# Kernel tuning notes

Measured on AMD Instinct MI355X. Metric: run time of the kernel, lower is better.

## Reference

```python
import jax, jax.numpy as jnp
import numpy as np

N_NODES = 100000
N_EDGES = 1000000
D = 64
HID = 64
OUT = 64
N_CLS = 10
N_GRAPHS = 512
BN_EPS = 1e-5


def setup_inputs() -> dict:
    key = jax.random.key(0)
    ks = jax.random.split(key, 16)
    inp = {
        "x": jax.random.normal(ks[0], (N_NODES, D), dtype=jnp.float32),
        "edge_index": jax.random.randint(ks[1], (2, N_EDGES), 0, N_NODES, dtype=jnp.int32),
        "batch": jnp.sort(jax.random.randint(ks[2], (N_NODES,), 0, N_GRAPHS, dtype=jnp.int32)),
    }
    def lin(k, fi, fo):
        lim = 1.0 / np.sqrt(fi)
        kw, kb = jax.random.split(k)
        return (jax.random.uniform(kw, (fi, fo), minval=-lim, maxval=lim, dtype=jnp.float32),
                jax.random.uniform(kb, (fo,), minval=-lim, maxval=lim, dtype=jnp.float32))
    # conv0 MLP([64,64,64]) with BN after first linear
    inp["w0a"], inp["b0a"] = lin(ks[3], D, HID)
    inp["g0"] = jnp.ones((HID,), jnp.float32); inp["be0"] = jnp.zeros((HID,), jnp.float32)
    inp["m0"] = jnp.zeros((HID,), jnp.float32); inp["v0"] = jnp.ones((HID,), jnp.float32)
    inp["w0b"], inp["b0b"] = lin(ks[4], HID, HID)
    # conv1 MLP([64,64,64])
    inp["w1a"], inp["b1a"] = lin(ks[5], HID, HID)
    inp["g1"] = jnp.ones((HID,), jnp.float32); inp["be1"] = jnp.zeros((HID,), jnp.float32)
    inp["m1"] = jnp.zeros((HID,), jnp.float32); inp["v1"] = jnp.ones((HID,), jnp.float32)
    inp["w1b"], inp["b1b"] = lin(ks[6], HID, OUT)
    # classifier
    inp["wc"], inp["bc"] = lin(ks[7], OUT, N_CLS)
    return inp


def _bn_eval(h, g, b, m, v):
    return (h - m) * jax.lax.rsqrt(v + BN_EPS) * g + b


def _mlp(h, wa, ba, g, be, m, v, wb, bb):
    # Linear -> BN -> ReLU -> (dropout eval=identity) -> Linear
    h = h @ wa + ba
    h = jax.nn.relu(_bn_eval(h, g, be, m, v))
    return h @ wb + bb


def _gin_conv(h, src, dst, wa, ba, g, be, m, v, wb, bb):
    # GINConv eps=0: mlp(x + sum_{j->i} x_j), messages scatter-added at dst
    agg = jax.ops.segment_sum(h[src], dst, num_segments=N_NODES)
    return _mlp(h + agg, wa, ba, g, be, m, v, wb, bb)


def reference(x, edge_index, batch,
              w0a, b0a, g0, be0, m0, v0, w0b, b0b,
              w1a, b1a, g1, be1, m1, v1, w1b, b1b,
              wc, bc):
    src, dst = edge_index[0], edge_index[1]
    h = _gin_conv(x, src, dst, w0a, b0a, g0, be0, m0, v0, w0b, b0b)
    h = jax.nn.relu(h)  # dropout is identity in eval
    h = _gin_conv(h, src, dst, w1a, b1a, g1, be1, m1, v1, w1b, b1b)
    # global mean pool over batch indices
    sums = jax.ops.segment_sum(h, batch, num_segments=N_GRAPHS)
    cnts = jax.ops.segment_sum(jnp.ones((h.shape[0],), h.dtype), batch, num_segments=N_GRAPHS)
    pooled = sums / jnp.maximum(cnts, 1.0)[:, None]
    return pooled @ wc + bc
```

## Files before the change

kernel.cpp:

```cpp
#include <hip/hip_runtime.h>

#define N_NODES 100000
#define N_EDGES 1000000
#define N_GRAPHS 512
#define N_CLS 10
#define BN_EPS 1e-5f

#define SCAN_NB 200
#define NTILES 1563

typedef _Float16 half8 __attribute__((ext_vector_type(8)));
typedef _Float16 half4v __attribute__((ext_vector_type(4)));
typedef float floatx4 __attribute__((ext_vector_type(4)));
typedef int intx4 __attribute__((ext_vector_type(4)));

__global__ __launch_bounds__(256) void prep_kernel(
    const float* __restrict__ x, _Float16* __restrict__ xh,
    const int* __restrict__ batch, const int* __restrict__ dstI,
    int* __restrict__ deg, int* __restrict__ rank,
    const float* __restrict__ w0a, const float* __restrict__ b0a,
    const float* __restrict__ g0, const float* __restrict__ be0,
    const float* __restrict__ m0, const float* __restrict__ v0,
    const float* __restrict__ w0b,
    const float* __restrict__ w1a, const float* __restrict__ b1a,
    const float* __restrict__ g1, const float* __restrict__ be1,
    const float* __restrict__ m1, const float* __restrict__ v1,
    const float* __restrict__ w1b,
    int* __restrict__ gstart,
    _Float16* __restrict__ wHi, _Float16* __restrict__ wLo,
    float* __restrict__ b1p0, float* __restrict__ b1p1) {
    const int gid = blockIdx.x * 256 + threadIdx.x;

    if (gid < 1600000) {
        float4 v = ((const float4*)x)[gid];
        half4v h = {(_Float16)v.x, (_Float16)v.y, (_Float16)v.z, (_Float16)v.w};
        ((half4v*)xh)[gid] = h;
    }

    if (gid < N_EDGES)
        rank[gid] = atomicAdd(&deg[dstI[gid]], 1);

    if (gid <= N_NODES) {
        int bcur = (gid < N_NODES) ? batch[gid] : N_GRAPHS;
        int bprev = (gid > 0) ? batch[gid - 1] : -1;
        for (int g = bprev + 1; g <= bcur; ++g) gstart[g] = gid;
    }

    if (gid < 16384) {
        const int e = gid & 4095, mat = gid >> 12;
        const int jj = e & 7, lane = (e >> 3) & 63, c = (e >> 9) & 3, k0 = (e >> 11) & 1;
        const int k = k0 * 32 + (lane >> 4) * 8 + jj;
        const int col = c * 16 + (lane & 15);
        float val;
        if (mat == 0)      val = w0a[k * 64 + col] * (rsqrtf(v0[col] + BN_EPS) * g0[col]);
        else if (mat == 1) val = w0b[k * 64 + col];
        else if (mat == 2) val = w1a[k * 64 + col] * (rsqrtf(v1[col] + BN_EPS) * g1[col]);
        else               val = w1b[k * 64 + col];
        _Float16 hi = (_Float16)val;
        wHi[gid] = hi;
        wLo[gid] = (_Float16)(val - (float)hi);
    }

    if (gid >= 16384 && gid < 16512) {
        int t = gid - 16384;
        if (t < 64) {
            float s = rsqrtf(v0[t] + BN_EPS) * g0[t];
            b1p0[t] = (b0a[t] - m0[t]) * s + be0[t];
        } else {
            t -= 64;
            float s = rsqrtf(v1[t] + BN_EPS) * g1[t];
            b1p1[t] = (b1a[t] - m1[t]) * s + be1[t];
        }
    }
}

__global__ __launch_bounds__(256) void scanA_kernel(const int* __restrict__ deg,
                                                    int* __restrict__ bsum) {
    __shared__ int sh[256];
    const int base = blockIdx.x * 512;
    const int t = threadIdx.x;
    int a = 0, b = 0;
    if (base + t < N_NODES) a = deg[base + t];
    if (base + 256 + t < N_NODES) b = deg[base + 256 + t];
    sh[t] = a + b;
    __syncthreads();
#pragma unroll
    for (int off = 128; off > 0; off >>= 1) {
        if (t < off) sh[t] += sh[t + off];
        __syncthreads();
    }
    if (t == 0) bsum[blockIdx.x] = sh[0];
}

__global__ __launch_bounds__(256) void scanC_kernel(const int* __restrict__ deg,
                                                    const int* __restrict__ bsum,
                                                    int* __restrict__ rowptr) {
    __shared__ int sh[256];
    __shared__ int sboff[256];
    const int base = blockIdx.x * 512;
    const int t = threadIdx.x;

    const int bv = (t < SCAN_NB) ? bsum[t] : 0;
    sboff[t] = bv;

    const int i0 = base + 2 * t, i1 = i0 + 1;
    const int d0 = (i0 < N_NODES) ? deg[i0] : 0;
    const int d1 = (i1 < N_NODES) ? deg[i1] : 0;
    const int p = d0 + d1;
    sh[t] = p;
    __syncthreads();
#pragma unroll
    for (int off = 1; off < 256; off <<= 1) {
        int u = (t >= off) ? sh[t - off] : 0;
        int ub = (t >= off) ? sboff[t - off] : 0;
        __syncthreads();
        sh[t] += u;
        sboff[t] += ub;
        __syncthreads();
    }
    const int myoff = (blockIdx.x == 0) ? 0 : sboff[blockIdx.x - 1];
    const int excl = myoff + sh[t] - p;
    if (i0 < N_NODES) rowptr[i0] = excl;
    if (i1 < N_NODES) rowptr[i1] = excl + d0;
    if (blockIdx.x == 0 && t == 0) rowptr[N_NODES] = N_EDGES;
}

__global__ __launch_bounds__(256) void fill_kernel(const intx4* __restrict__ srcI4,
                                                   const intx4* __restrict__ dstI4,
                                                   const intx4* __restrict__ rank4,
                                                   const int* __restrict__ rowptr,
                                                   int* __restrict__ sortedSrc) {
    int q = blockIdx.x * 256 + threadIdx.x;
    if (q >= N_EDGES / 4) return;
    intx4 s = __builtin_nontemporal_load(&srcI4[q]);
    intx4 d = __builtin_nontemporal_load(&dstI4[q]);
    intx4 r = __builtin_nontemporal_load(&rank4[q]);
    __builtin_nontemporal_store(s.x, &sortedSrc[rowptr[d.x] + r.x]);
    __builtin_nontemporal_store(s.y, &sortedSrc[rowptr[d.y] + r.y]);
    __builtin_nontemporal_store(s.z, &sortedSrc[rowptr[d.z] + r.z]);
    __builtin_nontemporal_store(s.w, &sortedSrc[rowptr[d.w] + r.w]);
}

template <int POOL>
__global__ __launch_bounds__(256) void conv_mfma(
    const _Float16* __restrict__ in, const int* __restrict__ rowptr,
    const int* __restrict__ srcList,
    const _Float16* __restrict__ wH1, const _Float16* __restrict__ wL1,
    const _Float16* __restrict__ wH2, const _Float16* __restrict__ wL2,
    const float* __restrict__ b1, const float* __restrict__ b2,
    _Float16* __restrict__ out, const int* __restrict__ batch,
    float* __restrict__ pooled) {
    __shared__ __align__(16) _Float16 scratch[4][2304];
    __shared__ float pooledLoc[8 * 64];
    __shared__ int bIds[64];
    __shared__ int maxSlot;

    const int tid = threadIdx.x;
    const int j = tid & 63, wv = tid >> 6;
    const int eoff = j >> 4;
    const int lf = j & 15;
    const int base = blockIdx.x * 64;
    const int strip0 = base + wv * 16;

    if (POOL) {
        pooledLoc[tid] = 0.f;
        pooledLoc[tid + 256] = 0.f;
        if (tid == 0) maxSlot = 0;
        if (j < 16) {
            int node = strip0 + j;
            bIds[wv * 16 + j] = (node < N_NODES) ? batch[node] : -1;
        }
    }

    const int rpv = rowptr[min(strip0 + min(j, 16), N_NODES)];

    _Float16* aggH = scratch[wv];
    _Float16* aggL = scratch[wv] + 1152;

    for (int mq = 0; mq < 4; ++mq) {
        const int m0 = mq * 4;
        int rr[5];
#pragma unroll
        for (int i = 0; i < 5; ++i) rr[i] = __builtin_amdgcn_readlane(rpv, m0 + i);
        int cnt[4];
#pragma unroll
        for (int i = 0; i < 4; ++i)
            cnt[i] = (strip0 + m0 + i < N_NODES) ? rr[i + 1] - rr[i] : 0;

        float aR[4][4];
#pragma unroll
        for (int i = 0; i < 4; ++i)
#pragma unroll
            for (int q = 0; q < 4; ++q) aR[i][q] = 0.f;

        half4v sS[4];
#pragma unroll
        for (int i = 0; i < 4; ++i) {
            sS[i] = (half4v){0, 0, 0, 0};
            if (eoff == 0 && strip0 + m0 + i < N_NODES)
                sS[i] = *(const half4v*)(in + (size_t)(strip0 + m0 + i) * 64 + lf * 4);
        }
        half4v vT[4][4];
#pragma unroll
        for (int i = 0; i < 4; ++i) {
            const int g = (min(cnt[i], 16) + 3) >> 2;
#pragma unroll
            for (int k = 0; k < 4; ++k) {
                vT[i][k] = (half4v){0, 0, 0, 0};
                if (k < g) {
                    int ec = min(4 * k + eoff, cnt[i] - 1);
                    int id = srcList[rr[i] + ec];
                    vT[i][k] = *(const half4v*)(in + (size_t)id * 64 + lf * 4);
                }
            }
        }
#pragma unroll
        for (int i = 0; i < 4; ++i) {
#pragma unroll
            for (int k = 0; k < 4; ++k) {
                if (4 * k + eoff < cnt[i]) {
                    aR[i][0] += (float)vT[i][k].x; aR[i][1] += (float)vT[i][k].y;
                    aR[i][2] += (float)vT[i][k].z; aR[i][3] += (float)vT[i][k].w;
                }
            }
        }
#pragma unroll
        for (int i = 0; i < 4; ++i) {
            for (int eb = 16; eb < cnt[i]; eb += 16) {
#pragma unroll
                for (int k = 0; k < 4; ++k) {
                    int e_ = eb + 4 * k + eoff;
                    if (e_ < cnt[i]) {
                        int id = srcList[rr[i] + e_];
                        half4v t = *(const half4v*)(in + (size_t)id * 64 + lf * 4);
                        aR[i][0] += (float)t.x; aR[i][1] += (float)t.y;
                        aR[i][2] += (float)t.z; aR[i][3] += (float)t.w;
                    }
                }
            }
        }
#pragma unroll
        for (int i = 0; i < 4; ++i) {
            if (eoff == 0) {
                aR[i][0] += (float)sS[i].x; aR[i][1] += (float)sS[i].y;
                aR[i][2] += (float)sS[i].z; aR[i][3] += (float)sS[i].w;
            }
#pragma unroll
            for (int q = 0; q < 4; ++q) {
                aR[i][q] += __shfl_xor(aR[i][q], 16, 64);
                aR[i][q] += __shfl_xor(aR[i][q], 32, 64);
            }
            if (j < 16) {
                half4v hi, lo;
#pragma unroll
                for (int q = 0; q < 4; ++q) {
                    hi[q] = (_Float16)aR[i][q];
                    lo[q] = (_Float16)(aR[i][q] - (float)hi[q]);
                }
                *(half4v*)(aggH + (m0 + i) * 72 + 4 * j) = hi;
                *(half4v*)(aggL + (m0 + i) * 72 + 4 * j) = lo;
            }
        }
    }

    const int l15 = j & 15, quad = j >> 4;
    const floatx4 vzero = {0.f, 0.f, 0.f, 0.f};

    floatx4 acc[4] = {vzero, vzero, vzero, vzero};
    {
        const _Float16* aH0 = aggH + l15 * 72 + quad * 8;
        const _Float16* aL0 = aggL + l15 * 72 + quad * 8;
#pragma unroll
        for (int k0 = 0; k0 < 2; ++k0) {
            half8 aH = *(const half8*)(aH0 + k0 * 32);
            half8 aL = *(const half8*)(aL0 + k0 * 32);
#pragma unroll
            for (int c = 0; c < 4; ++c) {
                const int fo = ((k0 * 4 + c) * 64 + j) * 8;
                half8 bH = *(const half8*)(wH1 + fo);
                half8 bL = *(const half8*)(wL1 + fo);
                acc[c] = __builtin_amdgcn_mfma_f32_16x16x32_f16(aH, bH, acc[c], 0, 0, 0);
                acc[c] = __builtin_amdgcn_mfma_f32_16x16x32_f16(aL, bH, acc[c], 0, 0, 0);
                acc[c] = __builtin_amdgcn_mfma_f32_16x16x32_f16(aH, bL, acc[c], 0, 0, 0);
            }
        }
    }
    _Float16* hH = aggH;
    _Float16* hL = aggL;
#pragma unroll
    for (int c = 0; c < 4; ++c) {
        const float bv = b1[c * 16 + l15];
#pragma unroll
        for (int r = 0; r < 4; ++r) {
            const int row = quad * 4 + r, col = c * 16 + l15;
            float v = acc[c][r] + bv;
            v = fmaxf(v, 0.f);
            const _Float16 hi = (_Float16)v;
            hH[row * 72 + col] = hi;
            hL[row * 72 + col] = (_Float16)(v - (float)hi);
        }
    }

    floatx4 acc2[4] = {vzero, vzero, vzero, vzero};
    {
        const _Float16* aH0 = hH + l15 * 72 + quad * 8;
        const _Float16* aL0 = hL + l15 * 72 + quad * 8;
#pragma unroll
        for (int k0 = 0; k0 < 2; ++k0) {
            half8 aH = *(const half8*)(aH0 + k0 * 32);
            half8 aL = *(const half8*)(aL0 + k0 * 32);
#pragma unroll
            for (int c = 0; c < 4; ++c) {
                const int fo = ((k0 * 4 + c) * 64 + j) * 8;
                half8 bH = *(const half8*)(wH2 + fo);
                half8 bL = *(const half8*)(wL2 + fo);
                acc2[c] = __builtin_amdgcn_mfma_f32_16x16x32_f16(aH, bH, acc2[c], 0, 0, 0);
                acc2[c] = __builtin_amdgcn_mfma_f32_16x16x32_f16(aL, bH, acc2[c], 0, 0, 0);
                acc2[c] = __builtin_amdgcn_mfma_f32_16x16x32_f16(aH, bL, acc2[c], 0, 0, 0);
            }
        }
    }

    if (!POOL) {
#pragma unroll
        for (int c = 0; c < 4; ++c) {
            const float bv = b2[c * 16 + l15];
#pragma unroll
            for (int r = 0; r < 4; ++r) {
                const int node = strip0 + quad * 4 + r;
                if (node < N_NODES)
                    out[(size_t)node * 64 + c * 16 + l15] =
                        (_Float16)fmaxf(acc2[c][r] + bv, 0.f);
            }
        }
    } else {
        float* oT = (float*)scratch[wv];
#pragma unroll
        for (int c = 0; c < 4; ++c) {
            const float bv = b2[c * 16 + l15];
#pragma unroll
            for (int r = 0; r < 4; ++r)
                oT[(quad * 4 + r) * 66 + c * 16 + l15] = acc2[c][r] + bv;
        }
        __syncthreads();
        const int b0 = bIds[0];
        int curB = -1;
        float accv = 0.f;
        for (int r = 0; r < 16; ++r) {
            const int b = bIds[wv * 16 + r];
            if (b < 0) break;
            const float v = oT[r * 66 + j];
            if (b != curB) {
                if (curB >= 0) {
                    const int s = curB - b0;
                    if (s >= 0 && s < 8) {
                        atomicAdd(&pooledLoc[s * 64 + j], accv);
                        if (j == 0) atomicMax(&maxSlot, s);
                    } else {
                        atomicAdd(&pooled[curB * 64 + j], accv);
                    }
                }
                curB = b;
                accv = v;
            } else {
                accv += v;
            }
        }
        if (curB >= 0) {
            const int s = curB - b0;
            if (s >= 0 && s < 8) {
                atomicAdd(&pooledLoc[s * 64 + j], accv);
                if (j == 0) atomicMax(&maxSlot, s);
            } else {
                atomicAdd(&pooled[curB * 64 + j], accv);
            }
        }
        __syncthreads();
        if (b0 >= 0) {
            const int ns = maxSlot + 1;
            for (int s = wv; s < ns; s += 4)
                atomicAdd(&pooled[(b0 + s) * 64 + j], pooledLoc[s * 64 + j]);
        }
    }
}

__global__ __launch_bounds__(64) void classifier_kernel(const float* __restrict__ pooled,
                                                        const int* __restrict__ gstart,
                                                        const float* __restrict__ wc,
                                                        const float* __restrict__ bc,
                                                        float* __restrict__ out) {
    const int g = blockIdx.x;
    const int j = threadIdx.x;
    const float c = fmaxf((float)(gstart[g + 1] - gstart[g]), 1.f);
    const float mean = pooled[g * 64 + j] / c;
#pragma unroll
    for (int cc = 0; cc < N_CLS; ++cc) {
        float p = mean * wc[j * N_CLS + cc];
#pragma unroll
        for (int off = 32; off > 0; off >>= 1) p += __shfl_down(p, off, 64);
        if (j == 0) out[g * N_CLS + cc] = p + bc[cc];
    }
}


extern "C" void kernel_launch(void* const* d_in, const int* in_sizes, int n_in,
                              void* d_out, int out_size, void* d_ws, size_t ws_size,
                              hipStream_t stream) {
    const float* x   = (const float*)d_in[0];
    const int*   ei  = (const int*)d_in[1];
    const int* batch = (const int*)d_in[2];
    const float* w0a = (const float*)d_in[3];
    const float* b0a = (const float*)d_in[4];
    const float* g0  = (const float*)d_in[5];
    const float* be0 = (const float*)d_in[6];
    const float* m0  = (const float*)d_in[7];
    const float* v0  = (const float*)d_in[8];
    const float* w0b = (const float*)d_in[9];
    const float* b0b = (const float*)d_in[10];
    const float* w1a = (const float*)d_in[11];
    const float* b1a = (const float*)d_in[12];
    const float* g1  = (const float*)d_in[13];
    const float* be1 = (const float*)d_in[14];
    const float* m1  = (const float*)d_in[15];
    const float* v1  = (const float*)d_in[16];
    const float* w1b = (const float*)d_in[17];
    const float* b1b = (const float*)d_in[18];
    const float* wc  = (const float*)d_in[19];
    const float* bc  = (const float*)d_in[20];
    float* out = (float*)d_out;

    const int* srcI = ei;
    const int* dstI = ei + N_EDGES;

    int* ws = (int*)d_ws;
    int*      deg       = ws;
    int*      bsum      = ws + 100000;
    float*    pooled    = (float*)(ws + 100404);
    int*      rowptr    = ws + 133172;
    int*      rank      = ws + 233176;
    int*      sortedSrc = ws + 1233176;
    _Float16* xh        = (_Float16*)(ws + 2233176);
    _Float16* h1        = (_Float16*)(ws + 5433176);
    float*    b1p0      = (float*)(ws + 8633176);
    float*    b1p1      = (float*)(ws + 8633240);
    int*      gstart    = ws + 8633304;
    _Float16* wHi       = (_Float16*)(ws + 8633820);
    _Float16* wLo       = (_Float16*)(ws + 8642012);

    (void)hipMemsetAsync((void*)deg, 0, 133172 * sizeof(int), stream);
    prep_kernel<<<6250, 256, 0, stream>>>(x, xh, batch, dstI, deg, rank,
                                          w0a, b0a, g0, be0, m0, v0, w0b,
                                          w1a, b1a, g1, be1, m1, v1, w1b,
                                          gstart, wHi, wLo, b1p0, b1p1);

    scanA_kernel<<<SCAN_NB, 256, 0, stream>>>(deg, bsum);
    scanC_kernel<<<SCAN_NB, 256, 0, stream>>>(deg, bsum, rowptr);
    fill_kernel<<<(N_EDGES / 4 + 255) / 256, 256, 0, stream>>>(
        (const intx4*)srcI, (const intx4*)dstI, (const intx4*)rank, rowptr, sortedSrc);

    conv_mfma<0><<<NTILES, 256, 0, stream>>>(xh, rowptr, sortedSrc,
                                             wHi, wLo, wHi + 4096, wLo + 4096,
                                             b1p0, b0b, h1, nullptr, nullptr);

    conv_mfma<1><<<NTILES, 256, 0, stream>>>(h1, rowptr, sortedSrc,
                                             wHi + 8192, wLo + 8192, wHi + 12288, wLo + 12288,
                                             b1p1, b1b, nullptr, batch, pooled);

    classifier_kernel<<<N_GRAPHS, 64, 0, stream>>>(pooled, gstart, wc, bc, out);
}
```

Before: 321.4 us.

## Halve conv block size to 128 threads and simplify edge fill kernel

The conv kernels now run two waves per block covering 32 nodes, launched over 3125 blocks, so 100000 nodes divide exactly. That lets all the node-bounds checks and sentinel handling be dropped. The fill kernel goes back to one edge per thread with plain scalar loads and stores instead of vectorized nontemporal ones. Smaller blocks are meant to improve scheduling granularity and occupancy, at the cost of more blocks and more pooled atomics per node.

```diff
diff --git a/kernel.cpp b/kernel.cpp
--- a/kernel.cpp
+++ b/kernel.cpp
@@ -7,12 +7,11 @@
 #define BN_EPS 1e-5f
 
 #define SCAN_NB 200
-#define NTILES 1563
+#define NTILES2 3125
 
 typedef _Float16 half8 __attribute__((ext_vector_type(8)));
 typedef _Float16 half4v __attribute__((ext_vector_type(4)));
 typedef float floatx4 __attribute__((ext_vector_type(4)));
-typedef int intx4 __attribute__((ext_vector_type(4)));
 
 __global__ __launch_bounds__(256) void prep_kernel(
     const float* __restrict__ x, _Float16* __restrict__ xh,
@@ -125,24 +124,18 @@
     if (blockIdx.x == 0 && t == 0) rowptr[N_NODES] = N_EDGES;
 }
 
-__global__ __launch_bounds__(256) void fill_kernel(const intx4* __restrict__ srcI4,
-                                                   const intx4* __restrict__ dstI4,
-                                                   const intx4* __restrict__ rank4,
+__global__ __launch_bounds__(256) void fill_kernel(const int* __restrict__ srcI,
+                                                   const int* __restrict__ dstI,
+                                                   const int* __restrict__ rank,
                                                    const int* __restrict__ rowptr,
                                                    int* __restrict__ sortedSrc) {
-    int q = blockIdx.x * 256 + threadIdx.x;
-    if (q >= N_EDGES / 4) return;
-    intx4 s = __builtin_nontemporal_load(&srcI4[q]);
-    intx4 d = __builtin_nontemporal_load(&dstI4[q]);
-    intx4 r = __builtin_nontemporal_load(&rank4[q]);
-    __builtin_nontemporal_store(s.x, &sortedSrc[rowptr[d.x] + r.x]);
-    __builtin_nontemporal_store(s.y, &sortedSrc[rowptr[d.y] + r.y]);
-    __builtin_nontemporal_store(s.z, &sortedSrc[rowptr[d.z] + r.z]);
-    __builtin_nontemporal_store(s.w, &sortedSrc[rowptr[d.w] + r.w]);
+    int e = blockIdx.x * 256 + threadIdx.x;
+    if (e >= N_EDGES) return;
+    sortedSrc[rowptr[dstI[e]] + rank[e]] = srcI[e];
 }
 
 template <int POOL>
-__global__ __launch_bounds__(256) void conv_mfma(
+__global__ __launch_bounds__(128) void conv_mfma(
     const _Float16* __restrict__ in, const int* __restrict__ rowptr,
     const int* __restrict__ srcList,
     const _Float16* __restrict__ wH1, const _Float16* __restrict__ wL1,
@@ -150,29 +143,26 @@
     const float* __restrict__ b1, const float* __restrict__ b2,
     _Float16* __restrict__ out, const int* __restrict__ batch,
     float* __restrict__ pooled) {
-    __shared__ __align__(16) _Float16 scratch[4][2304];
+    __shared__ __align__(16) _Float16 scratch[2][2304];
     __shared__ float pooledLoc[8 * 64];
-    __shared__ int bIds[64];
+    __shared__ int bIds[32];
     __shared__ int maxSlot;
 
     const int tid = threadIdx.x;
     const int j = tid & 63, wv = tid >> 6;
     const int eoff = j >> 4;
     const int lf = j & 15;
-    const int base = blockIdx.x * 64;
+    const int base = blockIdx.x * 32;
     const int strip0 = base + wv * 16;
 
     if (POOL) {
-        pooledLoc[tid] = 0.f;
-        pooledLoc[tid + 256] = 0.f;
+#pragma unroll
+        for (int q = 0; q < 4; ++q) pooledLoc[tid + q * 128] = 0.f;
         if (tid == 0) maxSlot = 0;
-        if (j < 16) {
-            int node = strip0 + j;
-            bIds[wv * 16 + j] = (node < N_NODES) ? batch[node] : -1;
-        }
-    }
-
-    const int rpv = rowptr[min(strip0 + min(j, 16), N_NODES)];
+        if (j < 16) bIds[wv * 16 + j] = batch[strip0 + j];
+    }
+
+    const int rpv = rowptr[strip0 + min(j, 16)];
 
     _Float16* aggH = scratch[wv];
     _Float16* aggL = scratch[wv] + 1152;
@@ -184,8 +174,7 @@
         for (int i = 0; i < 5; ++i) rr[i] = __builtin_amdgcn_readlane(rpv, m0 + i);
         int cnt[4];
 #pragma unroll
-        for (int i = 0; i < 4; ++i)
-            cnt[i] = (strip0 + m0 + i < N_NODES) ? rr[i + 1] - rr[i] : 0;
+        for (int i = 0; i < 4; ++i) cnt[i] = rr[i + 1] - rr[i];
 
         float aR[4][4];
 #pragma unroll
@@ -197,7 +186,7 @@
 #pragma unroll
         for (int i = 0; i < 4; ++i) {
             sS[i] = (half4v){0, 0, 0, 0};
-            if (eoff == 0 && strip0 + m0 + i < N_NODES)
+            if (eoff == 0)
                 sS[i] = *(const half4v*)(in + (size_t)(strip0 + m0 + i) * 64 + lf * 4);
         }
         half4v vT[4][4];
@@ -328,9 +317,8 @@
 #pragma unroll
             for (int r = 0; r < 4; ++r) {
                 const int node = strip0 + quad * 4 + r;
-                if (node < N_NODES)
-                    out[(size_t)node * 64 + c * 16 + l15] =
-                        (_Float16)fmaxf(acc2[c][r] + bv, 0.f);
+                out[(size_t)node * 64 + c * 16 + l15] =
+                    (_Float16)fmaxf(acc2[c][r] + bv, 0.f);
             }
         }
     } else {
@@ -348,7 +336,6 @@
         float accv = 0.f;
         for (int r = 0; r < 16; ++r) {
             const int b = bIds[wv * 16 + r];
-            if (b < 0) break;
             const float v = oT[r * 66 + j];
             if (b != curB) {
                 if (curB >= 0) {
@@ -366,7 +353,7 @@
                 accv += v;
             }
         }
-        if (curB >= 0) {
+        {
             const int s = curB - b0;
             if (s >= 0 && s < 8) {
                 atomicAdd(&pooledLoc[s * 64 + j], accv);
@@ -376,11 +363,9 @@
             }
         }
         __syncthreads();
-        if (b0 >= 0) {
-            const int ns = maxSlot + 1;
-            for (int s = wv; s < ns; s += 4)
-                atomicAdd(&pooled[(b0 + s) * 64 + j], pooledLoc[s * 64 + j]);
-        }
+        const int ns = maxSlot + 1;
+        for (int s = wv; s < ns; s += 2)
+            atomicAdd(&pooled[(b0 + s) * 64 + j], pooledLoc[s * 64 + j]);
     }
 }
 
@@ -455,16 +440,15 @@
 
     scanA_kernel<<<SCAN_NB, 256, 0, stream>>>(deg, bsum);
     scanC_kernel<<<SCAN_NB, 256, 0, stream>>>(deg, bsum, rowptr);
-    fill_kernel<<<(N_EDGES / 4 + 255) / 256, 256, 0, stream>>>(
-        (const intx4*)srcI, (const intx4*)dstI, (const intx4*)rank, rowptr, sortedSrc);
-
-    conv_mfma<0><<<NTILES, 256, 0, stream>>>(xh, rowptr, sortedSrc,
-                                             wHi, wLo, wHi + 4096, wLo + 4096,
-                                             b1p0, b0b, h1, nullptr, nullptr);
-
-    conv_mfma<1><<<NTILES, 256, 0, stream>>>(h1, rowptr, sortedSrc,
-                                             wHi + 8192, wLo + 8192, wHi + 12288, wLo + 12288,
-                                             b1p1, b1b, nullptr, batch, pooled);
+    fill_kernel<<<(N_EDGES + 255) / 256, 256, 0, stream>>>(srcI, dstI, rank, rowptr, sortedSrc);
+
+    conv_mfma<0><<<NTILES2, 128, 0, stream>>>(xh, rowptr, sortedSrc,
+                                              wHi, wLo, wHi + 4096, wLo + 4096,
+                                              b1p0, b0b, h1, nullptr, nullptr);
+
+    conv_mfma<1><<<NTILES2, 128, 0, stream>>>(h1, rowptr, sortedSrc,
+                                              wHi + 8192, wLo + 8192, wHi + 12288, wLo + 12288,
+                                              b1p1, b1b, nullptr, batch, pooled);
 
     classifier_kernel<<<N_GRAPHS, 64, 0, stream>>>(pooled, gstart, wc, bc, out);
 }
```

Measured after the change: 292.0 us. 9.1% less time.
